# Performance work log

Measured on AMD Instinct MI355X. Metric: run time of the kernel, lower is better.

The kernel has to match this reference:

```python
import jax, jax.numpy as jnp
import numpy as np

N, E = 30000, 480000          # nodes, edges (avg degree 16)
DIM, DQK, H = 128, 128, 8     # dim_in = dim_v = 128, dim_qk = 128, heads
FD = DQK // H                 # kernel feature dim per head
DVH = DIM // H                # value dim per head


def setup_inputs() -> dict:
    key = jax.random.key(0)
    ks = jax.random.split(key, 12)
    g = lambda k, shape: jax.random.normal(k, shape, jnp.float32)
    return {
        "x": g(ks[0], (N, DIM)),
        "vec": g(ks[1], (N, 3, DIM)) * 0.1,
        "edge_vec": g(ks[2], (E, 3)),
        "edge_weight": jax.random.uniform(ks[3], (N, 1), jnp.float32),
        "W_fc1": g(ks[4], (DIM, 2 * DQK + DIM)) / np.sqrt(DIM),
        "W_fcv": g(ks[5], (DIM, 3 * DIM)) / np.sqrt(DIM),
        "b_fcv": jnp.zeros((3 * DIM,), jnp.float32),
        "W_fco": g(ks[6], (DIM, DIM)) / np.sqrt(DIM),
        "b_fco": jnp.zeros((DIM,), jnp.float32),
        "W_out": g(ks[7], (DIM, 3 * DIM)) / np.sqrt(DIM),
        "W_vecproj": g(ks[8], (DIM, 3 * DIM)) / np.sqrt(DIM),
        "W_equiv": g(ks[9], (DIM, DIM)) / np.sqrt(DIM),
        "ln_scale": jnp.ones((DIM,), jnp.float32),
        "ln_bias": jnp.zeros((DIM,), jnp.float32),
        "edge_index": jax.random.randint(ks[10], (2, E), 0, N),
    }


def _phi(z):
    # positive kernel feature map (elu + 1), per head: [N, DQK] -> [N, H, FD]
    return jax.nn.elu(z.reshape(z.shape[0], H, FD)) + 1.0


def reference(x, vec, edge_vec, edge_weight,
              W_fc1, W_fcv, b_fcv, W_fco, b_fco, W_out, W_vecproj, W_equiv,
              ln_scale, ln_bias, edge_index):
    # fc_1 -> q | k | non-attention residual
    h1 = x @ W_fc1
    q, k, non_att = h1[:, :DQK], h1[:, DQK:2 * DQK], h1[:, 2 * DQK:]
    # fc_v -> v | vec1 gate | vec2 gate
    pv = x @ W_fcv + b_fcv
    v, vec1, vec2 = pv[:, :DIM], pv[:, DIM:2 * DIM], pv[:, 2 * DIM:]

    # kernelized linear self-attention over the node set (order 1->1)
    qf, kf = _phi(q), _phi(k)                      # [N,H,FD]
    vh = v.reshape(N, H, DVH)                      # [N,H,DVH]
    kv = jnp.einsum('nhf,nhd->hfd', kf, vh)        # [H,FD,DVH]
    z = kf.sum(0)                                  # [H,FD]
    num = jnp.einsum('nhf,hfd->nhd', qf, kv)
    den = jnp.einsum('nhf,hf->nh', qf, z)[..., None] + 1e-6
    att = (num / den).reshape(N, DIM)

    # equivariant vector projections: v1p, v2p, v3p
    vp = jnp.einsum('nci,io->nco', vec, W_vecproj)  # [N,3,3*DIM]
    v1p, v2p, v3p = vp[..., :DIM], vp[..., DIM:2 * DIM], vp[..., 2 * DIM:]
    vec_dot = (v1p * v2p).sum(1)                    # [N,DIM]

    # MPNN propagate: per-edge vector messages, scatter-sum to destination
    src, dst = edge_index[0], edge_index[1]
    msg = vec[src] * vec1[src][:, None, :] + edge_vec[:, :, None] * vec2[src][:, None, :]
    vec_agg = jax.ops.segment_sum(msg, dst, num_segments=N)  # [N,3,DIM]

    # gated output combination (o1, o2, o3)
    o = att @ W_out
    o1, o2, o3 = o[:, :DIM], o[:, DIM:2 * DIM], o[:, 2 * DIM:]
    delta_x = vec_dot * o2 + o3
    delta_vec = v3p * o1[:, None, :] + vec_agg

    att_out = ((att + delta_x) @ W_fco + b_fco) * edge_weight
    out_x = non_att + att_out

    # LayerNorm over channel dim, then equivariant projection
    mu = delta_vec.mean(-1, keepdims=True)
    var = delta_vec.var(-1, keepdims=True)
    dvn = (delta_vec - mu) / jnp.sqrt(var + 1e-5) * ln_scale + ln_bias
    out_vec = dvn @ W_equiv
    return out_x, out_vec
```

## Files before the change

### kernel.cpp

```cpp
#include <hip/hip_runtime.h>
#include <math.h>

#define NN 30000
#define EE 480000
#define DIM 128
#define KVB 512

typedef __attribute__((ext_vector_type(8))) short bf16x8;
typedef __attribute__((ext_vector_type(8))) short s16x8;
typedef __attribute__((ext_vector_type(4))) short s16x4;
typedef __attribute__((ext_vector_type(4))) float f32x4;
typedef __attribute__((ext_vector_type(4))) float float4v;
typedef unsigned short ushort_t;

__device__ inline short f2bf(float f) {
    union { float f; unsigned u; } v; v.f = f;
    unsigned u = v.u;
    u += 0x7fffu + ((u >> 16) & 1u);
    return (short)(u >> 16);
}
__device__ inline float bf2f(unsigned short u) {
    union { unsigned u; float f; } v; v.u = ((unsigned)u) << 16; return v.f;
}
__device__ inline unsigned pack2(float a, float b) {
    return (unsigned)(ushort_t)f2bf(a) | ((unsigned)(ushort_t)f2bf(b) << 16);
}

__device__ inline bf16x8 cvt8(float4v lo, float4v hi) {
    bf16x8 r;
    r[0] = f2bf(lo[0]); r[1] = f2bf(lo[1]); r[2] = f2bf(lo[2]); r[3] = f2bf(lo[3]);
    r[4] = f2bf(hi[0]); r[5] = f2bf(hi[1]); r[6] = f2bf(hi[2]); r[7] = f2bf(hi[3]);
    return r;
}
__device__ inline void bf8_to_f(bf16x8 v, float4v& lo, float4v& hi) {
#pragma unroll
    for (int i = 0; i < 4; ++i) {
        lo[i] = bf2f((unsigned short)v[i]);
        hi[i] = bf2f((unsigned short)v[4 + i]);
    }
}

__global__ void pack_all(const float* __restrict__ fc1, const float* __restrict__ fcv,
                         const float* __restrict__ wout, const float* __restrict__ wvp,
                         const float* __restrict__ fco, const float* __restrict__ weq,
                         short* __restrict__ Wpk) {
    int fid = blockIdx.x * 4 + (threadIdx.x >> 6);
    int lane = threadIdx.x & 63;
    const float* src; int Nsrc, c0, f;
    if (fid < 96)       { src = fc1;  Nsrc = 384; c0 = 0;   f = fid; }
    else if (fid < 192) { src = fcv;  Nsrc = 384; c0 = 0;   f = fid - 96; }
    else if (fid < 288) { src = wout; Nsrc = 384; c0 = 0;   f = fid - 192; }
    else if (fid < 352) { src = wvp;  Nsrc = 384; c0 = 0;   f = fid - 288; }
    else if (fid < 384) { src = wvp;  Nsrc = 384; c0 = 256; f = fid - 352; }
    else if (fid < 416) { src = fco;  Nsrc = 128; c0 = 0;   f = fid - 384; }
    else                { src = weq;  Nsrc = 128; c0 = 0;   f = fid - 416; }
    int ct = f >> 2, kk = f & 3;
    int k0 = kk * 32 + (lane >> 4) * 8;
    int col = c0 + ct * 16 + (lane & 15);
    bf16x8 v;
#pragma unroll
    for (int i = 0; i < 8; ++i) v[i] = f2bf(src[(size_t)(k0 + i) * Nsrc + col]);
    *(bf16x8*)(Wpk + ((size_t)fid * 64 + lane) * 8) = v;
}

template<int COLS, int CT_PER, bool BIAS, typename InT, typename OutT>
__global__ __launch_bounds__(256) void mfma_gemm(const InT* __restrict__ in,
        const short* __restrict__ Wpk, const float* __restrict__ bias,
        OutT* __restrict__ out, int nrows) {
    const int lane = threadIdx.x & 63;
    const int wid = threadIdx.x >> 6;
    const int rbase = blockIdx.x * 128 + wid * 32;
    if (rbase >= nrows) return;
    const int ct0 = blockIdx.y * CT_PER;
    const int rlo = lane & 15, khi = (lane >> 4) * 8;
    bf16x8 a[2][4];
#pragma unroll
    for (int t = 0; t < 2; ++t) {
        int row = min(rbase + t * 16 + rlo, nrows - 1);
        const InT* rp = in + (size_t)row * 128 + khi;
#pragma unroll
        for (int kk = 0; kk < 4; ++kk) {
            if constexpr (sizeof(InT) == 4) {
                float4v lo = *(const float4v*)(rp + kk * 32);
                float4v hi = *(const float4v*)(rp + kk * 32 + 4);
                a[t][kk] = cvt8(lo, hi);
            } else {
                a[t][kk] = *(const bf16x8*)(rp + kk * 32);
            }
        }
    }
#pragma unroll
    for (int c = 0; c < CT_PER; ++c) {
        const int ct = ct0 + c;
        bf16x8 b[4];
#pragma unroll
        for (int kk = 0; kk < 4; ++kk)
            b[kk] = *(const bf16x8*)(Wpk + ((size_t)(ct * 4 + kk) * 64 + lane) * 8);
        f32x4 acc0 = {0.f, 0.f, 0.f, 0.f}, acc1 = {0.f, 0.f, 0.f, 0.f};
#pragma unroll
        for (int kk = 0; kk < 4; ++kk) {
            acc0 = __builtin_amdgcn_mfma_f32_16x16x32_bf16(a[0][kk], b[kk], acc0, 0, 0, 0);
            acc1 = __builtin_amdgcn_mfma_f32_16x16x32_bf16(a[1][kk], b[kk], acc1, 0, 0, 0);
        }
        const int col = ct * 16 + rlo;
        const float bv = BIAS ? bias[col] : 0.f;
#pragma unroll
        for (int r = 0; r < 4; ++r) {
            int row0 = rbase + (lane >> 4) * 4 + r;
            int row1 = row0 + 16;
            if constexpr (sizeof(OutT) == 4) {
                if (row0 < nrows) out[(size_t)row0 * COLS + col] = acc0[r] + bv;
                if (row1 < nrows) out[(size_t)row1 * COLS + col] = acc1[r] + bv;
            } else {
                if (row0 < nrows) out[(size_t)row0 * COLS + col] = (OutT)f2bf(acc0[r] + bv);
                if (row1 < nrows) out[(size_t)row1 * COLS + col] = (OutT)f2bf(acc1[r] + bv);
            }
        }
    }
}

__global__ __launch_bounds__(256) void vp_gemm(const float* __restrict__ in,
        const short* __restrict__ Wpk, ushort_t* __restrict__ vp12,
        ushort_t* __restrict__ v3p, int nrows) {
    const int lane = threadIdx.x & 63;
    const int wid = threadIdx.x >> 6;
    const int rbase = blockIdx.x * 128 + wid * 32;
    if (rbase >= nrows) return;
    const int ct0 = blockIdx.y * 8;
    const int rlo = lane & 15, khi = (lane >> 4) * 8;
    bf16x8 a[2][4];
#pragma unroll
    for (int t = 0; t < 2; ++t) {
        int row = min(rbase + t * 16 + rlo, nrows - 1);
        const float* rp = in + (size_t)row * 128 + khi;
#pragma unroll
        for (int kk = 0; kk < 4; ++kk) {
            float4v lo = *(const float4v*)(rp + kk * 32);
            float4v hi = *(const float4v*)(rp + kk * 32 + 4);
            a[t][kk] = cvt8(lo, hi);
        }
    }
#pragma unroll
    for (int c = 0; c < 8; ++c) {
        const int ct = ct0 + c;
        bf16x8 b[4];
#pragma unroll
        for (int kk = 0; kk < 4; ++kk)
            b[kk] = *(const bf16x8*)(Wpk + ((size_t)(ct * 4 + kk) * 64 + lane) * 8);
        f32x4 acc0 = {0.f, 0.f, 0.f, 0.f}, acc1 = {0.f, 0.f, 0.f, 0.f};
#pragma unroll
        for (int kk = 0; kk < 4; ++kk) {
            acc0 = __builtin_amdgcn_mfma_f32_16x16x32_bf16(a[0][kk], b[kk], acc0, 0, 0, 0);
            acc1 = __builtin_amdgcn_mfma_f32_16x16x32_bf16(a[1][kk], b[kk], acc1, 0, 0, 0);
        }
        const int col = ct * 16 + rlo;
#pragma unroll
        for (int r = 0; r < 4; ++r) {
            int row0 = rbase + (lane >> 4) * 4 + r;
            int row1 = row0 + 16;
            if (col < 256) {
                if (row0 < nrows) vp12[(size_t)row0 * 256 + col] = (ushort_t)f2bf(acc0[r]);
                if (row1 < nrows) vp12[(size_t)row1 * 256 + col] = (ushort_t)f2bf(acc1[r]);
            } else {
                if (row0 < nrows) v3p[(size_t)row0 * 128 + col - 256] = (ushort_t)f2bf(acc0[r]);
                if (row1 < nrows) v3p[(size_t)row1 * 128 + col - 256] = (ushort_t)f2bf(acc1[r]);
            }
        }
    }
}

__global__ __launch_bounds__(256) void kv_part(const float* __restrict__ h1,
        const float* __restrict__ pv, float* __restrict__ slab) {
    __shared__ float kf_s[8][DIM];
    __shared__ float v_s[8][DIM];
    const int tid = threadIdx.x;
    const int rpb = (NN + KVB - 1) / KVB;
    const int n0 = blockIdx.x * rpb;
    const int n1 = min(n0 + rpb, NN);
    const int base = tid * 8;
    const int hf = base >> 4;
    const int h = hf >> 4;
    const int d0 = base & 15;
    const int lr = tid >> 5;
    const int lg = tid & 31;
    const bool isK = lg < 16;
    const int le = (lg & 15) * 8;
    float acc[8];
#pragma unroll
    for (int i = 0; i < 8; ++i) acc[i] = 0.f;
    float zacc = 0.f;
    float4v p0 = {0,0,0,0}, p1 = {0,0,0,0};
    bool pvalid = false;
    {
        int n = n0 + lr;
        pvalid = n < n1;
        if (pvalid) {
            const float* src = isK ? (h1 + (size_t)n * 384 + 128 + le)
                                   : (pv + (size_t)n * 384 + le);
            p0 = *(const float4v*)src;
            p1 = *(const float4v*)(src + 4);
        }
    }
    for (int nt = n0; nt < n1; nt += 8) {
        __syncthreads();
        float4v c0 = p0, c1 = p1;
        if (!pvalid) { c0 = {0,0,0,0}; c1 = {0,0,0,0}; }
        else if (isK) {
#pragma unroll
            for (int i = 0; i < 4; ++i) {
                c0[i] = c0[i] > 0.f ? c0[i] + 1.f : expf(c0[i]);
                c1[i] = c1[i] > 0.f ? c1[i] + 1.f : expf(c1[i]);
            }
        }
        float* dst = (isK ? kf_s[lr] : v_s[lr]) + le;
        *(float4v*)dst = c0;
        *(float4v*)(dst + 4) = c1;
        __syncthreads();
        {
            int n = nt + 8 + lr;
            pvalid = n < n1;
            if (pvalid) {
                const float* src = isK ? (h1 + (size_t)n * 384 + 128 + le)
                                       : (pv + (size_t)n * 384 + le);
                p0 = *(const float4v*)src;
                p1 = *(const float4v*)(src + 4);
            }
        }
#pragma unroll
        for (int r = 0; r < 8; ++r) {
            float kfv = kf_s[r][hf];
#pragma unroll
            for (int i = 0; i < 8; ++i) acc[i] = fmaf(kfv, v_s[r][h * 16 + d0 + i], acc[i]);
            if (tid < 128) zacc += kf_s[r][tid];
        }
    }
    float* row = slab + (size_t)blockIdx.x * 2176;
#pragma unroll
    for (int i = 0; i < 8; ++i) row[base + i] = acc[i];
    if (tid < 128) row[2048 + tid] = zacc;
}

__global__ void kv_final(const float* __restrict__ slab, float* __restrict__ kvz) {
    int i = blockIdx.x * 256 + threadIdx.x;
    if (i >= 2176) return;
    float a[8];
#pragma unroll
    for (int j = 0; j < 8; ++j) a[j] = 0.f;
    for (int b = 0; b < KVB; b += 8) {
#pragma unroll
        for (int j = 0; j < 8; ++j) a[j] += slab[(size_t)(b + j) * 2176 + i];
    }
    kvz[i] = ((a[0] + a[1]) + (a[2] + a[3])) + ((a[4] + a[5]) + (a[6] + a[7]));
}

__global__ void attn_apply(const float* __restrict__ h1, const float* __restrict__ kvz,
                           ushort_t* __restrict__ att) {
    __shared__ float kv_s[8 * 16 * 17];
    __shared__ float z_s[DIM];
    __shared__ float qf_s[8][DIM];
    const int tid = threadIdx.x;
    const int n0 = blockIdx.x * 8;
    for (int i = tid; i < 2048; i += 128) {
        int hf = i >> 4, d = i & 15;
        kv_s[hf * 17 + d] = kvz[i];
    }
    z_s[tid] = kvz[2048 + tid];
#pragma unroll
    for (int r = 0; r < 8; ++r) {
        float qv = h1[(size_t)(n0 + r) * 384 + tid];
        qf_s[r][tid] = qv > 0.f ? qv + 1.f : expf(qv);
    }
    __syncthreads();
    const int h = tid >> 4, d = tid & 15;
#pragma unroll
    for (int r = 0; r < 8; ++r) {
        float num = 0.f, den = 0.f;
#pragma unroll
        for (int f = 0; f < 16; ++f) {
            float q = qf_s[r][h * 16 + f];
            num = fmaf(q, kv_s[(h * 16 + f) * 17 + d], num);
            den = fmaf(q, z_s[h * 16 + f], den);
        }
        att[(size_t)(n0 + r) * DIM + tid] = (ushort_t)f2bf(num / (den + 1e-6f));
    }
}

__global__ __launch_bounds__(256) void vecdot_reduce(const ushort_t* __restrict__ vp12,
        const float* __restrict__ vec, const float* __restrict__ pv,
        ushort_t* __restrict__ vdot, ushort_t* __restrict__ P) {
    const int tid = threadIdx.x;
    const int c2 = tid & 63;
    const int sub = tid >> 6;
    const int n0 = blockIdx.x * 8;
#pragma unroll
    for (int rr = 0; rr < 2; ++rr) {
        const int n = n0 + sub + rr * 4;
        float a0 = 0.f, a1 = 0.f;
#pragma unroll
        for (int c = 0; c < 3; ++c) {
            unsigned u1 = *(const unsigned*)(vp12 + (size_t)(3 * n + c) * 256 + 2 * c2);
            unsigned u2 = *(const unsigned*)(vp12 + (size_t)(3 * n + c) * 256 + 128 + 2 * c2);
            a0 = fmaf(bf2f((unsigned short)u1), bf2f((unsigned short)u2), a0);
            a1 = fmaf(bf2f((unsigned short)(u1 >> 16)), bf2f((unsigned short)(u2 >> 16)), a1);
        }
        *(unsigned*)(vdot + (size_t)n * 128 + 2 * c2) = pack2(a0, a1);
        float2 v1 = *(const float2*)(pv + (size_t)n * 384 + 128 + 2 * c2);
        float2 v2 = *(const float2*)(pv + (size_t)n * 384 + 256 + 2 * c2);
        s16x8 pk;
        pk[0] = f2bf(v2.x);
        pk[4] = f2bf(v2.y);
#pragma unroll
        for (int c = 0; c < 3; ++c) {
            float2 vc = *(const float2*)(vec + ((size_t)n * 3 + c) * 128 + 2 * c2);
            pk[1 + c] = f2bf(vc.x * v1.x);
            pk[5 + c] = f2bf(vc.y * v1.y);
        }
        *(s16x8*)(P + (size_t)n * 512 + (size_t)c2 * 8) = pk;
    }
}

__global__ void hist_kernel(const int* __restrict__ eidx, int* __restrict__ cnt) {
    int e = blockIdx.x * 256 + threadIdx.x;
    if (e < EE) atomicAdd(&cnt[eidx[EE + e]], 1);
}

__global__ void scan_kernel(const int* __restrict__ cnt, int* __restrict__ off,
                            int* __restrict__ pos) {
    __shared__ int wsum[16];
    const int tid = threadIdx.x;
    const int lane = tid & 63, wv = tid >> 6;
    const int PER = 30;
    const int base = tid * PER;
    int local[PER];
    int s = 0;
#pragma unroll
    for (int i = 0; i < PER; ++i) {
        int idx = base + i;
        int c = (idx < NN) ? cnt[idx] : 0;
        local[i] = s;
        s += c;
    }
    int incl = s;
#pragma unroll
    for (int d = 1; d < 64; d <<= 1) {
        int v = __shfl_up(incl, d, 64);
        if (lane >= d) incl += v;
    }
    if (lane == 63) wsum[wv] = incl;
    __syncthreads();
    if (wv == 0 && lane < 16) {
        int v = wsum[lane];
        int iv = v;
#pragma unroll
        for (int d = 1; d < 16; d <<= 1) {
            int u = __shfl_up(iv, d, 16);
            if (lane >= d) iv += u;
        }
        wsum[lane] = iv - v;
    }
    __syncthreads();
    const int carry = wsum[wv] + (incl - s);
#pragma unroll
    for (int i = 0; i < PER; ++i) {
        int idx = base + i;
        if (idx < NN) {
            int v = carry + local[i];
            off[idx] = v;
            pos[idx] = v;
        }
    }
    if (tid == 1023) off[NN] = wsum[15] + incl;
}

__global__ void scatter_kernel(const int* __restrict__ eidx, const float* __restrict__ evec,
                               int* __restrict__ pos, int4* __restrict__ sorted4) {
    int e = blockIdx.x * 256 + threadIdx.x;
    if (e >= EE) return;
    int dst = eidx[EE + e];
    int src = eidx[e];
    float e0 = evec[(size_t)e * 3 + 0];
    float e1 = evec[(size_t)e * 3 + 1];
    float e2 = evec[(size_t)e * 3 + 2];
    int p = atomicAdd(&pos[dst], 1);
    sorted4[p] = make_int4(src, __float_as_int(e0), __float_as_int(e1), __float_as_int(e2));
}

__global__ __launch_bounds__(256) void edge_agg_kernel(
        const int* __restrict__ off, const int4* __restrict__ sorted4,
        const ushort_t* __restrict__ P, ushort_t* __restrict__ agg) {
    __shared__ int srcs[128];
    __shared__ float evs[3][128];
    __shared__ float part[3][128];
    const int dst = blockIdx.x;
    const int tid = threadIdx.x;
    const int g = tid >> 7, o = tid & 127;
    const int j0 = off[dst], j1 = off[dst + 1];
    float a0 = 0.f, a1 = 0.f, a2 = 0.f;
    for (int jt = j0; jt < j1; jt += 128) {
        const int m = min(128, j1 - jt);
        if (tid < m) {
            int4 w = sorted4[jt + tid];
            srcs[tid] = w.x;
            evs[0][tid] = __int_as_float(w.y);
            evs[1][tid] = __int_as_float(w.z);
            evs[2][tid] = __int_as_float(w.w);
        }
        __syncthreads();
        int jj = g;
        for (; jj + 14 < m; jj += 16) {
            s16x4 pk[8];
#pragma unroll
            for (int u = 0; u < 8; ++u)
                pk[u] = *(const s16x4*)(P + (size_t)srcs[jj + 2 * u] * 512 + o * 4);
#pragma unroll
            for (int u = 0; u < 8; ++u) {
                int e = jj + 2 * u;
                float v2 = bf2f((unsigned short)pk[u][0]);
                a0 += fmaf(evs[0][e], v2, bf2f((unsigned short)pk[u][1]));
                a1 += fmaf(evs[1][e], v2, bf2f((unsigned short)pk[u][2]));
                a2 += fmaf(evs[2][e], v2, bf2f((unsigned short)pk[u][3]));
            }
        }
        for (; jj < m; jj += 2) {
            s16x4 pk = *(const s16x4*)(P + (size_t)srcs[jj] * 512 + o * 4);
            float v2 = bf2f((unsigned short)pk[0]);
            a0 += fmaf(evs[0][jj], v2, bf2f((unsigned short)pk[1]));
            a1 += fmaf(evs[1][jj], v2, bf2f((unsigned short)pk[2]));
            a2 += fmaf(evs[2][jj], v2, bf2f((unsigned short)pk[3]));
        }
        __syncthreads();
    }
    if (g == 1) { part[0][o] = a0; part[1][o] = a1; part[2][o] = a2; }
    __syncthreads();
    if (g == 0) {
        a0 += part[0][o]; a1 += part[1][o]; a2 += part[2][o];
        agg[((size_t)dst * 3 + 0) * DIM + o] = (ushort_t)f2bf(a0);
        agg[((size_t)dst * 3 + 1) * DIM + o] = (ushort_t)f2bf(a1);
        agg[((size_t)dst * 3 + 2) * DIM + o] = (ushort_t)f2bf(a2);
    }
}

__global__ __launch_bounds__(256) void outx_mfma(const ushort_t* __restrict__ att,
        const ushort_t* __restrict__ vdot, const ushort_t* __restrict__ o,
        const short* __restrict__ Wpk, const float* __restrict__ bfco,
        const float* __restrict__ h1, const float* __restrict__ ew,
        float* __restrict__ outx) {
    const int lane = threadIdx.x & 63;
    const int wid = threadIdx.x >> 6;
    const int rbase = blockIdx.x * 128 + wid * 32;
    if (rbase >= NN) return;
    const int ct0 = blockIdx.y * 4;
    const int rlo = lane & 15, khi = (lane >> 4) * 8;
    bf16x8 a[2][4];
#pragma unroll
    for (int t = 0; t < 2; ++t) {
        int row = min(rbase + t * 16 + rlo, NN - 1);
        const ushort_t* pa = att + (size_t)row * 128 + khi;
        const ushort_t* pd = vdot + (size_t)row * 128 + khi;
        const ushort_t* po = o + (size_t)row * 384 + khi;
#pragma unroll
        for (int kk = 0; kk < 4; ++kk) {
            int kb = kk * 32;
            float4v al, ah, dl, dh, o2l, o2h, o3l, o3h;
            bf8_to_f(*(const bf16x8*)(pa + kb), al, ah);
            bf8_to_f(*(const bf16x8*)(pd + kb), dl, dh);
            bf8_to_f(*(const bf16x8*)(po + 128 + kb), o2l, o2h);
            bf8_to_f(*(const bf16x8*)(po + 256 + kb), o3l, o3h);
            a[t][kk] = cvt8(al + dl * o2l + o3l, ah + dh * o2h + o3h);
        }
    }
    float ewv[2][4];
#pragma unroll
    for (int t = 0; t < 2; ++t)
#pragma unroll
        for (int r = 0; r < 4; ++r)
            ewv[t][r] = ew[min(rbase + t * 16 + (lane >> 4) * 4 + r, NN - 1)];
#pragma unroll
    for (int c = 0; c < 4; ++c) {
        const int ct = ct0 + c;
        bf16x8 b[4];
#pragma unroll
        for (int kk = 0; kk < 4; ++kk)
            b[kk] = *(const bf16x8*)(Wpk + ((size_t)(ct * 4 + kk) * 64 + lane) * 8);
        f32x4 acc0 = {0.f, 0.f, 0.f, 0.f}, acc1 = {0.f, 0.f, 0.f, 0.f};
#pragma unroll
        for (int kk = 0; kk < 4; ++kk) {
            acc0 = __builtin_amdgcn_mfma_f32_16x16x32_bf16(a[0][kk], b[kk], acc0, 0, 0, 0);
            acc1 = __builtin_amdgcn_mfma_f32_16x16x32_bf16(a[1][kk], b[kk], acc1, 0, 0, 0);
        }
        const int col = ct * 16 + rlo;
        const float bv = bfco[col];
#pragma unroll
        for (int r = 0; r < 4; ++r) {
            int row0 = rbase + (lane >> 4) * 4 + r;
            if (row0 < NN)
                outx[(size_t)row0 * 128 + col] =
                    h1[(size_t)row0 * 384 + 256 + col] + (acc0[r] + bv) * ewv[0][r];
            int row1 = row0 + 16;
            if (row1 < NN)
                outx[(size_t)row1 * 128 + col] =
                    h1[(size_t)row1 * 384 + 256 + col] + (acc1[r] + bv) * ewv[1][r];
        }
    }
}

__global__ __launch_bounds__(256) void outvec_ln(const ushort_t* __restrict__ v3p,
        const ushort_t* __restrict__ o, const ushort_t* __restrict__ agg,
        const float* __restrict__ ln_scale, const float* __restrict__ ln_bias,
        ushort_t* __restrict__ dvn) {
    const int tid = threadIdx.x;
    const int c2 = tid & 63;
    const int row = blockIdx.x * 4 + (tid >> 6);
    const int n = row / 3;
    unsigned uv3 = *(const unsigned*)(v3p + (size_t)row * 128 + 2 * c2);
    unsigned uo1 = *(const unsigned*)(o + (size_t)n * 384 + 2 * c2);
    unsigned uag = *(const unsigned*)(agg + (size_t)row * 128 + 2 * c2);
    float dv0 = fmaf(bf2f((unsigned short)uv3), bf2f((unsigned short)uo1),
                     bf2f((unsigned short)uag));
    float dv1 = fmaf(bf2f((unsigned short)(uv3 >> 16)), bf2f((unsigned short)(uo1 >> 16)),
                     bf2f((unsigned short)(uag >> 16)));
    float s = dv0 + dv1;
    float s2 = fmaf(dv0, dv0, dv1 * dv1);
#pragma unroll
    for (int d = 1; d < 64; d <<= 1) {
        s += __shfl_xor(s, d, 64);
        s2 += __shfl_xor(s2, d, 64);
    }
    float mu = s * (1.f / 128.f);
    float rstd = rsqrtf(s2 * (1.f / 128.f) - mu * mu + 1e-5f);
    float r0 = fmaf((dv0 - mu) * rstd, ln_scale[2 * c2], ln_bias[2 * c2]);
    float r1 = fmaf((dv1 - mu) * rstd, ln_scale[2 * c2 + 1], ln_bias[2 * c2 + 1]);
    *(unsigned*)(dvn + (size_t)row * 128 + 2 * c2) = pack2(r0, r1);
}

extern "C" void kernel_launch(void* const* d_in, const int* in_sizes, int n_in,
                              void* d_out, int out_size, void* d_ws, size_t ws_size,
                              hipStream_t stream) {
    const float* x          = (const float*)d_in[0];
    const float* vec        = (const float*)d_in[1];
    const float* edge_vec   = (const float*)d_in[2];
    const float* edge_weight= (const float*)d_in[3];
    const float* W_fc1      = (const float*)d_in[4];
    const float* W_fcv      = (const float*)d_in[5];
    const float* b_fcv      = (const float*)d_in[6];
    const float* W_fco      = (const float*)d_in[7];
    const float* b_fco      = (const float*)d_in[8];
    const float* W_out      = (const float*)d_in[9];
    const float* W_vecproj  = (const float*)d_in[10];
    const float* W_equiv    = (const float*)d_in[11];
    const float* ln_scale   = (const float*)d_in[12];
    const float* ln_bias    = (const float*)d_in[13];
    const int*   edge_index = (const int*)d_in[14];

    float* out_x   = (float*)d_out;
    float* out_vec = out_x + (size_t)NN * DIM;
    ushort_t* Pb = (ushort_t*)d_out;

    float* ws   = (float*)d_ws;
    float* h1   = ws;
    float* pv   = h1 + 11520000;
    ushort_t* att_b  = (ushort_t*)(pv + 11520000);
    ushort_t* vdot_b = att_b + 3840000;
    ushort_t* o_b    = vdot_b + 3840000;
    ushort_t* agg_b  = o_b + 11520000;
    ushort_t* v3p_b  = agg_b + 11520000;
    float* kvz  = (float*)(v3p_b + 11520000);
    ushort_t* vp12_b = o_b;
    float* slab = (float*)o_b;
    ushort_t* dvn_b = (ushort_t*)pv;
    int* cnt    = (int*)(kvz + 2176);
    int* off    = cnt + NN;
    int* pos    = off + NN + 1;
    size_t soff = ((size_t)(pos + NN - (int*)ws) + 3) & ~(size_t)3;
    int4* sorted4 = (int4*)((int*)ws + soff);
    short* Wpk  = (short*)((int*)ws + soff + (size_t)4 * EE);
    short* pk_fc1  = Wpk;
    short* pk_fcv  = Wpk + 96 * 512;
    short* pk_wout = Wpk + 192 * 512;
    short* pk_vp   = Wpk + 288 * 512;
    short* pk_fco  = Wpk + 384 * 512;
    short* pk_weq  = Wpk + 416 * 512;

    hipMemsetAsync(cnt, 0, NN * sizeof(int), stream);

    pack_all<<<112, 256, 0, stream>>>(W_fc1, W_fcv, W_out, W_vecproj, W_fco, W_equiv, Wpk);

    hist_kernel<<<(EE + 255) / 256, 256, 0, stream>>>(edge_index, cnt);
    scan_kernel<<<1, 1024, 0, stream>>>(cnt, off, pos);
    scatter_kernel<<<(EE + 255) / 256, 256, 0, stream>>>(edge_index, edge_vec, pos, sorted4);

    const int gN = (NN + 127) / 128;
    const int g3N = (3 * NN + 127) / 128;
    mfma_gemm<384, 8, false, float, float><<<dim3(gN, 3), 256, 0, stream>>>(x, pk_fc1, nullptr, h1, NN);
    mfma_gemm<384, 8, true, float, float><<<dim3(gN, 3), 256, 0, stream>>>(x, pk_fcv, b_fcv, pv, NN);
    kv_part<<<KVB, 256, 0, stream>>>(h1, pv, slab);
    kv_final<<<9, 256, 0, stream>>>(slab, kvz);
    attn_apply<<<NN / 8, 128, 0, stream>>>(h1, kvz, att_b);
    vp_gemm<<<dim3(g3N, 3), 256, 0, stream>>>(vec, pk_vp, vp12_b, v3p_b, 3 * NN);
    vecdot_reduce<<<NN / 8, 256, 0, stream>>>(vp12_b, vec, pv, vdot_b, Pb);
    mfma_gemm<384, 8, false, ushort_t, ushort_t><<<dim3(gN, 3), 256, 0, stream>>>(att_b, pk_wout, nullptr, o_b, NN);
    edge_agg_kernel<<<NN, 256, 0, stream>>>(off, sorted4, Pb, agg_b);
    outx_mfma<<<dim3(gN, 2), 256, 0, stream>>>(att_b, vdot_b, o_b, pk_fco, b_fco, h1, edge_weight, out_x);
    outvec_ln<<<(3 * NN) / 4, 256, 0, stream>>>(v3p_b, o_b, agg_b, ln_scale, ln_bias, dvn_b);
    mfma_gemm<128, 4, false, ushort_t, float><<<dim3(g3N, 2), 256, 0, stream>>>(dvn_b, pk_weq, nullptr, out_vec, 3 * NN);
}
```

Before: 446.4 us.

## Store h1/pv in bf16, fuse fc1/fcv GEMMs, single-pass vp and equiv GEMMs

The h1 and pv intermediates are now stored as bf16 instead of fp32, which halves their write and read traffic in kv_part, attn_apply, vecdot_reduce and outx_mfma. The fc1 and fcv GEMMs are merged into one launch. vp_gemm now loops over all 24 column tiles in a single block, and the W_equiv GEMM covers all columns per block, so input rows are read and converted once rather than per column block. The trade-off is lower precision in q, k, v and the non-attention residual, plus less grid parallelism in the vp and equiv GEMMs.

```diff
diff --git a/kernel.cpp b/kernel.cpp
--- a/kernel.cpp
+++ b/kernel.cpp
@@ -63,6 +63,55 @@
     *(bf16x8*)(Wpk + ((size_t)fid * 64 + lane) * 8) = v;
 }
 
+__global__ __launch_bounds__(256) void x_gemm(const float* __restrict__ in,
+        const short* __restrict__ Wpk, const float* __restrict__ bfcv,
+        ushort_t* __restrict__ h1, ushort_t* __restrict__ pv, int nrows) {
+    const int lane = threadIdx.x & 63;
+    const int wid = threadIdx.x >> 6;
+    const int rbase = blockIdx.x * 128 + wid * 32;
+    if (rbase >= nrows) return;
+    const bool isPv = blockIdx.y >= 3;
+    const int ct0 = (blockIdx.y - (isPv ? 3 : 0)) * 8;
+    const short* W = Wpk + (isPv ? 96 * 512 : 0);
+    ushort_t* out = isPv ? pv : h1;
+    const int rlo = lane & 15, khi = (lane >> 4) * 8;
+    bf16x8 a[2][4];
+#pragma unroll
+    for (int t = 0; t < 2; ++t) {
+        int row = min(rbase + t * 16 + rlo, nrows - 1);
+        const float* rp = in + (size_t)row * 128 + khi;
+#pragma unroll
+        for (int kk = 0; kk < 4; ++kk) {
+            float4v lo = *(const float4v*)(rp + kk * 32);
+            float4v hi = *(const float4v*)(rp + kk * 32 + 4);
+            a[t][kk] = cvt8(lo, hi);
+        }
+    }
+#pragma unroll
+    for (int c = 0; c < 8; ++c) {
+        const int ct = ct0 + c;
+        bf16x8 b[4];
+#pragma unroll
+        for (int kk = 0; kk < 4; ++kk)
+            b[kk] = *(const bf16x8*)(W + ((size_t)(ct * 4 + kk) * 64 + lane) * 8);
+        f32x4 acc0 = {0.f, 0.f, 0.f, 0.f}, acc1 = {0.f, 0.f, 0.f, 0.f};
+#pragma unroll
+        for (int kk = 0; kk < 4; ++kk) {
+            acc0 = __builtin_amdgcn_mfma_f32_16x16x32_bf16(a[0][kk], b[kk], acc0, 0, 0, 0);
+            acc1 = __builtin_amdgcn_mfma_f32_16x16x32_bf16(a[1][kk], b[kk], acc1, 0, 0, 0);
+        }
+        const int col = ct * 16 + rlo;
+        const float bv = isPv ? bfcv[col] : 0.f;
+#pragma unroll
+        for (int r = 0; r < 4; ++r) {
+            int row0 = rbase + (lane >> 4) * 4 + r;
+            int row1 = row0 + 16;
+            if (row0 < nrows) out[(size_t)row0 * 384 + col] = (ushort_t)f2bf(acc0[r] + bv);
+            if (row1 < nrows) out[(size_t)row1 * 384 + col] = (ushort_t)f2bf(acc1[r] + bv);
+        }
+    }
+}
+
 template<int COLS, int CT_PER, bool BIAS, typename InT, typename OutT>
 __global__ __launch_bounds__(256) void mfma_gemm(const InT* __restrict__ in,
         const short* __restrict__ Wpk, const float* __restrict__ bias,
@@ -126,7 +175,6 @@
     const int wid = threadIdx.x >> 6;
     const int rbase = blockIdx.x * 128 + wid * 32;
     if (rbase >= nrows) return;
-    const int ct0 = blockIdx.y * 8;
     const int rlo = lane & 15, khi = (lane >> 4) * 8;
     bf16x8 a[2][4];
 #pragma unroll
@@ -140,9 +188,7 @@
             a[t][kk] = cvt8(lo, hi);
         }
     }
-#pragma unroll
-    for (int c = 0; c < 8; ++c) {
-        const int ct = ct0 + c;
+    for (int ct = 0; ct < 24; ++ct) {
         bf16x8 b[4];
 #pragma unroll
         for (int kk = 0; kk < 4; ++kk)
@@ -169,8 +215,8 @@
     }
 }
 
-__global__ __launch_bounds__(256) void kv_part(const float* __restrict__ h1,
-        const float* __restrict__ pv, float* __restrict__ slab) {
+__global__ __launch_bounds__(256) void kv_part(const ushort_t* __restrict__ h1,
+        const ushort_t* __restrict__ pv, float* __restrict__ slab) {
     __shared__ float kf_s[8][DIM];
     __shared__ float v_s[8][DIM];
     const int tid = threadIdx.x;
@@ -189,41 +235,37 @@
 #pragma unroll
     for (int i = 0; i < 8; ++i) acc[i] = 0.f;
     float zacc = 0.f;
-    float4v p0 = {0,0,0,0}, p1 = {0,0,0,0};
+    s16x8 praw = {0,0,0,0,0,0,0,0};
     bool pvalid = false;
     {
         int n = n0 + lr;
         pvalid = n < n1;
         if (pvalid) {
-            const float* src = isK ? (h1 + (size_t)n * 384 + 128 + le)
-                                   : (pv + (size_t)n * 384 + le);
-            p0 = *(const float4v*)src;
-            p1 = *(const float4v*)(src + 4);
+            const ushort_t* src = isK ? (h1 + (size_t)n * 384 + 128 + le)
+                                      : (pv + (size_t)n * 384 + le);
+            praw = *(const s16x8*)src;
         }
     }
     for (int nt = n0; nt < n1; nt += 8) {
         __syncthreads();
-        float4v c0 = p0, c1 = p1;
-        if (!pvalid) { c0 = {0,0,0,0}; c1 = {0,0,0,0}; }
-        else if (isK) {
-#pragma unroll
-            for (int i = 0; i < 4; ++i) {
-                c0[i] = c0[i] > 0.f ? c0[i] + 1.f : expf(c0[i]);
-                c1[i] = c1[i] > 0.f ? c1[i] + 1.f : expf(c1[i]);
-            }
+        float v8[8];
+#pragma unroll
+        for (int i = 0; i < 8; ++i) v8[i] = pvalid ? bf2f((unsigned short)praw[i]) : 0.f;
+        if (pvalid && isK) {
+#pragma unroll
+            for (int i = 0; i < 8; ++i) v8[i] = v8[i] > 0.f ? v8[i] + 1.f : expf(v8[i]);
         }
         float* dst = (isK ? kf_s[lr] : v_s[lr]) + le;
-        *(float4v*)dst = c0;
-        *(float4v*)(dst + 4) = c1;
+#pragma unroll
+        for (int i = 0; i < 8; ++i) dst[i] = v8[i];
         __syncthreads();
         {
             int n = nt + 8 + lr;
             pvalid = n < n1;
             if (pvalid) {
-                const float* src = isK ? (h1 + (size_t)n * 384 + 128 + le)
-                                       : (pv + (size_t)n * 384 + le);
-                p0 = *(const float4v*)src;
-                p1 = *(const float4v*)(src + 4);
+                const ushort_t* src = isK ? (h1 + (size_t)n * 384 + 128 + le)
+                                          : (pv + (size_t)n * 384 + le);
+                praw = *(const s16x8*)src;
             }
         }
 #pragma unroll
@@ -253,7 +295,7 @@
     kvz[i] = ((a[0] + a[1]) + (a[2] + a[3])) + ((a[4] + a[5]) + (a[6] + a[7]));
 }
 
-__global__ void attn_apply(const float* __restrict__ h1, const float* __restrict__ kvz,
+__global__ void attn_apply(const ushort_t* __restrict__ h1, const float* __restrict__ kvz,
                            ushort_t* __restrict__ att) {
     __shared__ float kv_s[8 * 16 * 17];
     __shared__ float z_s[DIM];
@@ -267,7 +309,7 @@
     z_s[tid] = kvz[2048 + tid];
 #pragma unroll
     for (int r = 0; r < 8; ++r) {
-        float qv = h1[(size_t)(n0 + r) * 384 + tid];
+        float qv = bf2f(h1[(size_t)(n0 + r) * 384 + tid]);
         qf_s[r][tid] = qv > 0.f ? qv + 1.f : expf(qv);
     }
     __syncthreads();
@@ -286,7 +328,7 @@
 }
 
 __global__ __launch_bounds__(256) void vecdot_reduce(const ushort_t* __restrict__ vp12,
-        const float* __restrict__ vec, const float* __restrict__ pv,
+        const float* __restrict__ vec, const ushort_t* __restrict__ pv,
         ushort_t* __restrict__ vdot, ushort_t* __restrict__ P) {
     const int tid = threadIdx.x;
     const int c2 = tid & 63;
@@ -304,16 +346,17 @@
             a1 = fmaf(bf2f((unsigned short)(u1 >> 16)), bf2f((unsigned short)(u2 >> 16)), a1);
         }
         *(unsigned*)(vdot + (size_t)n * 128 + 2 * c2) = pack2(a0, a1);
-        float2 v1 = *(const float2*)(pv + (size_t)n * 384 + 128 + 2 * c2);
-        float2 v2 = *(const float2*)(pv + (size_t)n * 384 + 256 + 2 * c2);
+        unsigned uv1 = *(const unsigned*)(pv + (size_t)n * 384 + 128 + 2 * c2);
+        unsigned uv2 = *(const unsigned*)(pv + (size_t)n * 384 + 256 + 2 * c2);
+        float v1x = bf2f((unsigned short)uv1), v1y = bf2f((unsigned short)(uv1 >> 16));
         s16x8 pk;
-        pk[0] = f2bf(v2.x);
-        pk[4] = f2bf(v2.y);
+        pk[0] = (short)(ushort_t)(uv2 & 0xffffu);
+        pk[4] = (short)(ushort_t)(uv2 >> 16);
 #pragma unroll
         for (int c = 0; c < 3; ++c) {
             float2 vc = *(const float2*)(vec + ((size_t)n * 3 + c) * 128 + 2 * c2);
-            pk[1 + c] = f2bf(vc.x * v1.x);
-            pk[5 + c] = f2bf(vc.y * v1.y);
+            pk[1 + c] = f2bf(vc.x * v1x);
+            pk[5 + c] = f2bf(vc.y * v1y);
         }
         *(s16x8*)(P + (size_t)n * 512 + (size_t)c2 * 8) = pk;
     }
@@ -443,7 +486,7 @@
 __global__ __launch_bounds__(256) void outx_mfma(const ushort_t* __restrict__ att,
         const ushort_t* __restrict__ vdot, const ushort_t* __restrict__ o,
         const short* __restrict__ Wpk, const float* __restrict__ bfco,
-        const float* __restrict__ h1, const float* __restrict__ ew,
+        const ushort_t* __restrict__ h1, const float* __restrict__ ew,
         float* __restrict__ outx) {
     const int lane = threadIdx.x & 63;
     const int wid = threadIdx.x >> 6;
@@ -495,11 +538,11 @@
             int row0 = rbase + (lane >> 4) * 4 + r;
             if (row0 < NN)
                 outx[(size_t)row0 * 128 + col] =
-                    h1[(size_t)row0 * 384 + 256 + col] + (acc0[r] + bv) * ewv[0][r];
+                    bf2f(h1[(size_t)row0 * 384 + 256 + col]) + (acc0[r] + bv) * ewv[0][r];
             int row1 = row0 + 16;
             if (row1 < NN)
                 outx[(size_t)row1 * 128 + col] =
-                    h1[(size_t)row1 * 384 + 256 + col] + (acc1[r] + bv) * ewv[1][r];
+                    bf2f(h1[(size_t)row1 * 384 + 256 + col]) + (acc1[r] + bv) * ewv[1][r];
         }
     }
 }
@@ -557,9 +600,9 @@
     ushort_t* Pb = (ushort_t*)d_out;
 
     float* ws   = (float*)d_ws;
-    float* h1   = ws;
-    float* pv   = h1 + 11520000;
-    ushort_t* att_b  = (ushort_t*)(pv + 11520000);
+    ushort_t* h1_b   = (ushort_t*)ws;
+    ushort_t* pv_b   = h1_b + 11520000;
+    ushort_t* att_b  = pv_b + 11520000;
     ushort_t* vdot_b = att_b + 3840000;
     ushort_t* o_b    = vdot_b + 3840000;
     ushort_t* agg_b  = o_b + 11520000;
@@ -567,7 +610,7 @@
     float* kvz  = (float*)(v3p_b + 11520000);
     ushort_t* vp12_b = o_b;
     float* slab = (float*)o_b;
-    ushort_t* dvn_b = (ushort_t*)pv;
+    ushort_t* dvn_b = pv_b;
     int* cnt    = (int*)(kvz + 2176);
     int* off    = cnt + NN;
     int* pos    = off + NN + 1;
@@ -575,7 +618,6 @@
     int4* sorted4 = (int4*)((int*)ws + soff);
     short* Wpk  = (short*)((int*)ws + soff + (size_t)4 * EE);
     short* pk_fc1  = Wpk;
-    short* pk_fcv  = Wpk + 96 * 512;
     short* pk_wout = Wpk + 192 * 512;
     short* pk_vp   = Wpk + 288 * 512;
     short* pk_fco  = Wpk + 384 * 512;
@@ -591,16 +633,15 @@
 
     const int gN = (NN + 127) / 128;
     const int g3N = (3 * NN + 127) / 128;
-    mfma_gemm<384, 8, false, float, float><<<dim3(gN, 3), 256, 0, stream>>>(x, pk_fc1, nullptr, h1, NN);
-    mfma_gemm<384, 8, true, float, float><<<dim3(gN, 3), 256, 0, stream>>>(x, pk_fcv, b_fcv, pv, NN);
-    kv_part<<<KVB, 256, 0, stream>>>(h1, pv, slab);
+    x_gemm<<<dim3(gN, 6), 256, 0, stream>>>(x, pk_fc1, b_fcv, h1_b, pv_b, NN);
+    kv_part<<<KVB, 256, 0, stream>>>(h1_b, pv_b, slab);
     kv_final<<<9, 256, 0, stream>>>(slab, kvz);
-    attn_apply<<<NN / 8, 128, 0, stream>>>(h1, kvz, att_b);
-    vp_gemm<<<dim3(g3N, 3), 256, 0, stream>>>(vec, pk_vp, vp12_b, v3p_b, 3 * NN);
-    vecdot_reduce<<<NN / 8, 256, 0, stream>>>(vp12_b, vec, pv, vdot_b, Pb);
+    attn_apply<<<NN / 8, 128, 0, stream>>>(h1_b, kvz, att_b);
+    vp_gemm<<<g3N, 256, 0, stream>>>(vec, pk_vp, vp12_b, v3p_b, 3 * NN);
+    vecdot_reduce<<<NN / 8, 256, 0, stream>>>(vp12_b, vec, pv_b, vdot_b, Pb);
     mfma_gemm<384, 8, false, ushort_t, ushort_t><<<dim3(gN, 3), 256, 0, stream>>>(att_b, pk_wout, nullptr, o_b, NN);
     edge_agg_kernel<<<NN, 256, 0, stream>>>(off, sorted4, Pb, agg_b);
-    outx_mfma<<<dim3(gN, 2), 256, 0, stream>>>(att_b, vdot_b, o_b, pk_fco, b_fco, h1, edge_weight, out_x);
+    outx_mfma<<<dim3(gN, 2), 256, 0, stream>>>(att_b, vdot_b, o_b, pk_fco, b_fco, h1_b, edge_weight, out_x);
     outvec_ln<<<(3 * NN) / 4, 256, 0, stream>>>(v3p_b, o_b, agg_b, ln_scale, ln_bias, dvn_b);
-    mfma_gemm<128, 4, false, ushort_t, float><<<dim3(g3N, 2), 256, 0, stream>>>(dvn_b, pk_weq, nullptr, out_vec, 3 * NN);
-}
+    mfma_gemm<128, 8, false, ushort_t, float><<<g3N, 256, 0, stream>>>(dvn_b, pk_weq, nullptr, out_vec, 3 * NN);
+}
```

Result: faster. 399.4 us (-10.5%).
